# Optimization experiments

Hardware: AMD Instinct MI355X
Metric: run time of the kernel (lower is better)

The kernel has to match this reference:

```python
import jax, jax.numpy as jnp
import numpy as np

H = 4
D = 64          # attention_head_size
HID = H * D     # 256
LN_EPS = 1e-12


def setup_inputs() -> dict:
    key = jax.random.key(0)
    ks = jax.random.split(key, 20)
    B, S = 8, 200
    s = 0.02
    inp = {
        'input_tensor': jax.random.normal(ks[0], (B, S, HID), jnp.float32),
        'attention_mask': jnp.zeros((B, 1, S, S), jnp.float32),
        'absolute_pos_K': jax.random.normal(ks[1], (B, S, HID), jnp.float32),
        'absolute_pos_V': jax.random.normal(ks[2], (B, S, HID), jnp.float32),
        'time_matrix_emb_K': jax.random.normal(ks[3], (B, S, S, HID), jnp.float32),
        'time_matrix_emb_V': jax.random.normal(ks[4], (B, S, S, HID), jnp.float32),
        'Wq': jax.random.normal(ks[5], (HID, HID), jnp.float32) * s,
        'bq': jnp.zeros((HID,), jnp.float32),
        'Wk': jax.random.normal(ks[6], (HID, HID), jnp.float32) * s,
        'bk': jnp.zeros((HID,), jnp.float32),
        'Wv': jax.random.normal(ks[7], (HID, HID), jnp.float32) * s,
        'bv': jnp.zeros((HID,), jnp.float32),
        'order_w': jax.random.normal(ks[8], (2 * D,), jnp.float32) * s,
        'order_b': jnp.zeros((), jnp.float32),
        'dist_w': jax.random.normal(ks[9], (2 * D,), jnp.float32) * s,
        'dist_b': jnp.zeros((), jnp.float32),
        'scalar': jax.random.normal(ks[10], (1,), jnp.float32),
        'Wd': jax.random.normal(ks[11], (HID, HID), jnp.float32) * s,
        'bd': jnp.zeros((HID,), jnp.float32),
        'ln_g': jnp.ones((HID,), jnp.float32),
        'ln_b': jnp.zeros((HID,), jnp.float32),
    }
    return inp


def _forward(input_tensor, attention_mask, absolute_pos_K, absolute_pos_V,
             time_matrix_emb_K, time_matrix_emb_V,
             Wq, bq, Wk, bk, Wv, bv, order_w, order_b, dist_w, dist_b,
             scalar, Wd, bd, ln_g, ln_b):
    B, S, _ = input_tensor.shape
    heads = lambda x: x.reshape(B, S, H, D).transpose(0, 2, 1, 3)  # -> [B,H,S,D]
    q = heads(input_tensor @ Wq + bq)
    k = heads(input_tensor @ Wk + bk)
    v = heads(input_tensor @ Wv + bv)
    posK = heads(absolute_pos_K)                                   # [B,H,S,D]
    posV = heads(absolute_pos_V)
    timeK = time_matrix_emb_K.reshape(B, S, S, H, D).transpose(0, 3, 1, 2, 4)  # [B,H,S,S,D]
    timeV = time_matrix_emb_V.reshape(B, S, S, H, D).transpose(0, 3, 1, 2, 4)

    scores = (jnp.einsum('bhid,bhjd->bhij', q, k)
              + jnp.einsum('bhid,bhjd->bhij', q, posK)
              + jnp.einsum('bhijd,bhid->bhij', timeK, q))          # [B,H,S,S]

    # order_affine(cat(q_i,k_j)) == q_i@w[:D] + k_j@w[D:] + b (Linear on concat)
    pr_order = jax.nn.sigmoid(jnp.einsum('bhid,d->bhi', q, order_w[:D])[:, :, :, None]
                              + jnp.einsum('bhjd,d->bhj', k, order_w[D:])[:, :, None, :]
                              + order_b)
    gd_order = jnp.triu(jnp.ones((S, S), jnp.float32), 1)[None, None]
    error_order = (jnp.log(pr_order + 1e-24) * gd_order
                   + jnp.log(1.0 - pr_order + 1e-24) * (1.0 - gd_order))

    idx = jnp.arange(S, dtype=jnp.float32)
    gd_dist = jnp.log(jnp.abs(idx[None, :] - idx[:, None]) + 1.0)[None, None]
    pr_dist = (jnp.einsum('bhid,d->bhi', q, dist_w[:D])[:, :, :, None]
               + jnp.einsum('bhjd,d->bhj', k, dist_w[D:])[:, :, None, :]
               + dist_b)
    error_distance = -jnp.square(gd_dist - pr_dist) * jnp.square(scalar[0]) / 2.0

    scores = scores + error_order + error_distance
    probs = jax.nn.softmax(scores / np.sqrt(D) + attention_mask, axis=-1)

    ctx = (jnp.einsum('bhij,bhjd->bhid', probs, v)
           + jnp.einsum('bhij,bhjd->bhid', probs, posV)
           + jnp.einsum('bhij,bhijd->bhid', probs, timeV))
    ctx = ctx.transpose(0, 2, 1, 3).reshape(B, S, HID)

    hs = ctx @ Wd + bd + input_tensor
    mu = jnp.mean(hs, axis=-1, keepdims=True)
    var = jnp.mean(jnp.square(hs - mu), axis=-1, keepdims=True)
    return (hs - mu) / jnp.sqrt(var + LN_EPS) * ln_g + ln_b


def reference(input_tensor, attention_mask, absolute_pos_K, absolute_pos_V,
              time_matrix_emb_K, time_matrix_emb_V,
              Wq, bq, Wk, bk, Wv, bv, order_w, order_b, dist_w, dist_b,
              scalar, Wd, bd, ln_g, ln_b):
    return _forward(input_tensor, attention_mask, absolute_pos_K, absolute_pos_V,
                    time_matrix_emb_K, time_matrix_emb_V,
                    Wq, bq, Wk, bk, Wv, bv, order_w, order_b, dist_w, dist_b,
                    scalar, Wd, bd, ln_g, ln_b)
```

## Files before the change

kernel.cpp:

```cpp
#include <hip/hip_runtime.h>

#define SB 8
#define SS 200
#define HID 256
#define NH 4
#define DH 64

__global__ __launch_bounds__(256) void proj_kernel(
    const float* __restrict__ in,
    const float* __restrict__ Wq, const float* __restrict__ bq,
    const float* __restrict__ Wk, const float* __restrict__ bk,
    const float* __restrict__ Wv, const float* __restrict__ bv,
    const float* __restrict__ posK, const float* __restrict__ posV,
    float* __restrict__ q_out, float* __restrict__ k_out,
    float* __restrict__ kpk_out, float* __restrict__ vpv_out)
{
    const int which = blockIdx.y;
    const float* W = (which == 0) ? Wq : (which == 1) ? Wk : Wv;
    const float* bias = (which == 0) ? bq : (which == 1) ? bk : bv;
    const int row0 = blockIdx.x * 16;
    __shared__ float sin_[16][HID];
    const int t = threadIdx.x;
    for (int r = 0; r < 16; r++)
        sin_[r][t] = in[(size_t)(row0 + r) * HID + t];
    __syncthreads();
    const int tx = t & 63, ty = t >> 6;
    const int c0 = tx * 4, r0 = ty * 4;
    float acc[4][4] = {};
    for (int kk = 0; kk < HID; kk++) {
        const float4 wv4 = *(const float4*)(W + (size_t)kk * HID + c0);
        float a[4];
        #pragma unroll
        for (int r = 0; r < 4; r++) a[r] = sin_[r0 + r][kk];
        #pragma unroll
        for (int r = 0; r < 4; r++) {
            acc[r][0] += a[r] * wv4.x;
            acc[r][1] += a[r] * wv4.y;
            acc[r][2] += a[r] * wv4.z;
            acc[r][3] += a[r] * wv4.w;
        }
    }
    const float4 b4 = *(const float4*)(bias + c0);
    #pragma unroll
    for (int r = 0; r < 4; r++) {
        const size_t off = (size_t)(row0 + r0 + r) * HID + c0;
        float4 o;
        o.x = acc[r][0] + b4.x;
        o.y = acc[r][1] + b4.y;
        o.z = acc[r][2] + b4.z;
        o.w = acc[r][3] + b4.w;
        if (which == 0) {
            *(float4*)(q_out + off) = o;
        } else if (which == 1) {
            *(float4*)(k_out + off) = o;
            const float4 p4 = *(const float4*)(posK + off);
            float4 s;
            s.x = o.x + p4.x; s.y = o.y + p4.y;
            s.z = o.z + p4.z; s.w = o.w + p4.w;
            *(float4*)(kpk_out + off) = s;
        } else {
            const float4 p4 = *(const float4*)(posV + off);
            float4 s;
            s.x = o.x + p4.x; s.y = o.y + p4.y;
            s.z = o.z + p4.z; s.w = o.w + p4.w;
            *(float4*)(vpv_out + off) = s;
        }
    }
}

__global__ __launch_bounds__(64) void rowdots_kernel(
    const float* __restrict__ q, const float* __restrict__ k,
    const float* __restrict__ order_w, const float* __restrict__ dist_w,
    float* __restrict__ qo, float* __restrict__ ko,
    float* __restrict__ qd, float* __restrict__ kd)
{
    const int row = blockIdx.x;
    const int l = threadIdx.x;
    const float ow1 = order_w[l], ow2 = order_w[64 + l];
    const float dw1 = dist_w[l],  dw2 = dist_w[64 + l];
    for (int h = 0; h < NH; h++) {
        const float qe = q[(size_t)row * HID + h * DH + l];
        const float ke = k[(size_t)row * HID + h * DH + l];
        float a = qe * ow1, b = ke * ow2, c = qe * dw1, d = ke * dw2;
        #pragma unroll
        for (int m = 32; m >= 1; m >>= 1) {
            a += __shfl_xor(a, m, 64);
            b += __shfl_xor(b, m, 64);
            c += __shfl_xor(c, m, 64);
            d += __shfl_xor(d, m, 64);
        }
        if (l == 0) {
            qo[row * NH + h] = a;
            ko[row * NH + h] = b;
            qd[row * NH + h] = c;
            kd[row * NH + h] = d;
        }
    }
}

__global__ __launch_bounds__(256) void attn_kernel(
    const float* __restrict__ q, const float* __restrict__ kpk,
    const float* __restrict__ vpv,
    const float* __restrict__ timeK, const float* __restrict__ timeV,
    const float* __restrict__ mask,
    const float* __restrict__ qo, const float* __restrict__ ko,
    const float* __restrict__ qd, const float* __restrict__ kd,
    const float* __restrict__ order_b_p, const float* __restrict__ dist_b_p,
    const float* __restrict__ scalar_p,
    float* __restrict__ ctx)
{
    const int blk = blockIdx.x;
    const int b = blk / SS, i = blk - b * SS;
    const int t = threadIdx.x;
    const int w = t >> 6, l = t & 63;
    const int h = l >> 4;
    const int sub = l & 15;

    __shared__ float sh_q[HID];
    __shared__ float sh_s[NH][SS + 8];
    __shared__ float sh_red[4][HID];

    const size_t rowq = (size_t)blk * HID;
    sh_q[t] = q[rowq + t];
    __syncthreads();

    const int d0 = l * 4;
    const float4 qr = *(const float4*)(sh_q + d0);

    const float qo_h = qo[blk * NH + h];
    const float qd_h = qd[blk * NH + h];
    const float order_b = *order_b_p;
    const float dist_b = *dist_b_p;
    const float sc = *scalar_p;
    const float sc2h = 0.5f * sc * sc;
    const size_t tb = (size_t)blk * SS;

    for (int j0 = 0; j0 < SS; j0 += 4) {
        const int j = j0 + w;
        const float4 tk = *(const float4*)(timeK + (tb + j) * (size_t)HID + d0);
        const float4 kk = *(const float4*)(kpk + ((size_t)(b * SS + j)) * HID + d0);
        float part = (tk.x + kk.x) * qr.x + (tk.y + kk.y) * qr.y
                   + (tk.z + kk.z) * qr.z + (tk.w + kk.w) * qr.w;
        part += __shfl_xor(part, 1, 64);
        part += __shfl_xor(part, 2, 64);
        part += __shfl_xor(part, 4, 64);
        part += __shfl_xor(part, 8, 64);
        if (sub == 0) {
            const float ko_jh = ko[(b * SS + j) * NH + h];
            const float kd_jh = kd[(b * SS + j) * NH + h];
            const float xo = qo_h + ko_jh + order_b;
            const float pr = 1.0f / (1.0f + __expf(-xo));
            const float eo = (j > i) ? __logf(pr + 1e-24f) : __logf(1.0f - pr + 1e-24f);
            const float xd = qd_h + kd_jh + dist_b;
            const float gd = __logf(fabsf((float)(i - j)) + 1.0f);
            const float dd = gd - xd;
            const float ed = -dd * dd * sc2h;
            const float mk = mask[tb + j];
            sh_s[h][j] = (part + eo + ed) * 0.125f + mk;
        }
    }
    __syncthreads();

    {
        float vals[4];
        float m = -1e30f;
        #pragma unroll
        for (int rep = 0; rep < 4; rep++) {
            const int j = l + rep * 64;
            vals[rep] = (j < SS) ? sh_s[w][j] : -1e30f;
            m = fmaxf(m, vals[rep]);
        }
        #pragma unroll
        for (int mm = 32; mm >= 1; mm >>= 1) m = fmaxf(m, __shfl_xor(m, mm, 64));
        float sum = 0.0f;
        float es[4];
        #pragma unroll
        for (int rep = 0; rep < 4; rep++) {
            const int j = l + rep * 64;
            if (j < SS) { es[rep] = __expf(vals[rep] - m); sum += es[rep]; }
        }
        #pragma unroll
        for (int mm = 32; mm >= 1; mm >>= 1) sum += __shfl_xor(sum, mm, 64);
        const float inv = 1.0f / sum;
        #pragma unroll
        for (int rep = 0; rep < 4; rep++) {
            const int j = l + rep * 64;
            if (j < SS) sh_s[w][j] = es[rep] * inv;
        }
    }
    __syncthreads();

    float4 acc = make_float4(0.f, 0.f, 0.f, 0.f);
    for (int j0 = 0; j0 < SS; j0 += 4) {
        const int j = j0 + w;
        const float4 tv = *(const float4*)(timeV + (tb + j) * (size_t)HID + d0);
        const float4 vv = *(const float4*)(vpv + ((size_t)(b * SS + j)) * HID + d0);
        const float p = sh_s[h][j];
        acc.x += p * (tv.x + vv.x);
        acc.y += p * (tv.y + vv.y);
        acc.z += p * (tv.z + vv.z);
        acc.w += p * (tv.w + vv.w);
    }
    *(float4*)(&sh_red[w][d0]) = acc;
    __syncthreads();
    ctx[rowq + t] = sh_red[0][t] + sh_red[1][t] + sh_red[2][t] + sh_red[3][t];
}

__global__ __launch_bounds__(256) void outproj_kernel(
    const float* __restrict__ ctx, const float* __restrict__ Wd,
    const float* __restrict__ bd, const float* __restrict__ input,
    float* __restrict__ hs)
{
    const int row0 = blockIdx.x * 16;
    __shared__ float sin_[16][HID];
    const int t = threadIdx.x;
    for (int r = 0; r < 16; r++)
        sin_[r][t] = ctx[(size_t)(row0 + r) * HID + t];
    __syncthreads();
    const int tx = t & 63, ty = t >> 6;
    const int c0 = tx * 4, r0 = ty * 4;
    float acc[4][4] = {};
    for (int kk = 0; kk < HID; kk++) {
        const float4 wv4 = *(const float4*)(Wd + (size_t)kk * HID + c0);
        float a[4];
        #pragma unroll
        for (int r = 0; r < 4; r++) a[r] = sin_[r0 + r][kk];
        #pragma unroll
        for (int r = 0; r < 4; r++) {
            acc[r][0] += a[r] * wv4.x;
            acc[r][1] += a[r] * wv4.y;
            acc[r][2] += a[r] * wv4.z;
            acc[r][3] += a[r] * wv4.w;
        }
    }
    const float4 b4 = *(const float4*)(bd + c0);
    #pragma unroll
    for (int r = 0; r < 4; r++) {
        const size_t off = (size_t)(row0 + r0 + r) * HID + c0;
        const float4 i4 = *(const float4*)(input + off);
        float4 o;
        o.x = acc[r][0] + b4.x + i4.x;
        o.y = acc[r][1] + b4.y + i4.y;
        o.z = acc[r][2] + b4.z + i4.z;
        o.w = acc[r][3] + b4.w + i4.w;
        *(float4*)(hs + off) = o;
    }
}

__global__ __launch_bounds__(256) void ln_kernel(
    const float* __restrict__ hs, const float* __restrict__ g,
    const float* __restrict__ be, float* __restrict__ out)
{
    const int row = blockIdx.x;
    const int t = threadIdx.x;
    const int w = t >> 6, l = t & 63;
    __shared__ float red[4];
    const float v = hs[(size_t)row * HID + t];
    float s = v;
    #pragma unroll
    for (int m = 32; m >= 1; m >>= 1) s += __shfl_xor(s, m, 64);
    if (l == 0) red[w] = s;
    __syncthreads();
    const float mu = (red[0] + red[1] + red[2] + red[3]) * (1.0f / 256.0f);
    __syncthreads();
    const float d = v - mu;
    float s2 = d * d;
    #pragma unroll
    for (int m = 32; m >= 1; m >>= 1) s2 += __shfl_xor(s2, m, 64);
    if (l == 0) red[w] = s2;
    __syncthreads();
    const float var = (red[0] + red[1] + red[2] + red[3]) * (1.0f / 256.0f);
    out[(size_t)row * HID + t] = d * rsqrtf(var + 1e-12f) * g[t] + be[t];
}

extern "C" void kernel_launch(void* const* d_in, const int* in_sizes, int n_in,
                              void* d_out, int out_size, void* d_ws, size_t ws_size,
                              hipStream_t stream) {
    const float* input   = (const float*)d_in[0];
    const float* mask    = (const float*)d_in[1];
    const float* posK    = (const float*)d_in[2];
    const float* posV    = (const float*)d_in[3];
    const float* timeK   = (const float*)d_in[4];
    const float* timeV   = (const float*)d_in[5];
    const float* Wq      = (const float*)d_in[6];
    const float* bq      = (const float*)d_in[7];
    const float* Wk      = (const float*)d_in[8];
    const float* bk      = (const float*)d_in[9];
    const float* Wv      = (const float*)d_in[10];
    const float* bv      = (const float*)d_in[11];
    const float* order_w = (const float*)d_in[12];
    const float* order_b = (const float*)d_in[13];
    const float* dist_w  = (const float*)d_in[14];
    const float* dist_b  = (const float*)d_in[15];
    const float* scalar  = (const float*)d_in[16];
    const float* Wd      = (const float*)d_in[17];
    const float* bd      = (const float*)d_in[18];
    const float* ln_g    = (const float*)d_in[19];
    const float* ln_b    = (const float*)d_in[20];

    const int NROW = SB * SS;
    float* ws = (float*)d_ws;
    float* q_ws   = ws;
    float* k_ws   = q_ws   + 409600;
    float* kpk_ws = k_ws   + 409600;
    float* vpv_ws = kpk_ws + 409600;
    float* qo_ws  = vpv_ws + 409600;
    float* ko_ws  = qo_ws  + 6400;
    float* qd_ws  = ko_ws  + 6400;
    float* kd_ws  = qd_ws  + 6400;
    float* ctx_ws = kd_ws  + 6400;
    float* hs_ws  = ctx_ws + 409600;

    proj_kernel<<<dim3(NROW / 16, 3), 256, 0, stream>>>(
        input, Wq, bq, Wk, bk, Wv, bv, posK, posV,
        q_ws, k_ws, kpk_ws, vpv_ws);
    rowdots_kernel<<<NROW, 64, 0, stream>>>(
        q_ws, k_ws, order_w, dist_w, qo_ws, ko_ws, qd_ws, kd_ws);
    attn_kernel<<<NROW, 256, 0, stream>>>(
        q_ws, kpk_ws, vpv_ws, timeK, timeV, mask,
        qo_ws, ko_ws, qd_ws, kd_ws, order_b, dist_b, scalar, ctx_ws);
    outproj_kernel<<<NROW / 16, 256, 0, stream>>>(
        ctx_ws, Wd, bd, input, hs_ws);
    ln_kernel<<<NROW, 256, 0, stream>>>(
        hs_ws, ln_g, ln_b, (float*)d_out);
}
```

Measured before the change: 742.2 us.

## Fuse rowdots into projection and out-proj plus layernorm into attention

Folds the order/distance row-dot reductions into the QKV projection epilogue and folds the output projection, residual and layer norm into the attention kernel, cutting five launches to two and removing intermediate buffers. Per-key order/distance error terms are precomputed into shared memory before the score loop. The time-embedding streams use nontemporal loads and the key loops are unrolled by two for more loads in flight. The fused per-row output projection rereads Wd from cache in every block, which adds some compute per block.

```diff
diff --git a/kernel.cpp b/kernel.cpp
--- a/kernel.cpp
+++ b/kernel.cpp
@@ -6,58 +6,102 @@
 #define NH 4
 #define DH 64
 
-__global__ __launch_bounds__(256) void proj_kernel(
+typedef float f32x4_t __attribute__((ext_vector_type(4)));
+
+__device__ __forceinline__ float4 ntload4(const float* p) {
+    f32x4_t v = __builtin_nontemporal_load((const f32x4_t*)p);
+    return make_float4(v.x, v.y, v.z, v.w);
+}
+
+__global__ __launch_bounds__(256) void proj_fused_kernel(
     const float* __restrict__ in,
     const float* __restrict__ Wq, const float* __restrict__ bq,
     const float* __restrict__ Wk, const float* __restrict__ bk,
     const float* __restrict__ Wv, const float* __restrict__ bv,
     const float* __restrict__ posK, const float* __restrict__ posV,
-    float* __restrict__ q_out, float* __restrict__ k_out,
-    float* __restrict__ kpk_out, float* __restrict__ vpv_out)
+    const float* __restrict__ order_w, const float* __restrict__ dist_w,
+    float* __restrict__ q_out, float* __restrict__ kpk_out,
+    float* __restrict__ vpv_out,
+    float* __restrict__ qo, float* __restrict__ ko,
+    float* __restrict__ qd, float* __restrict__ kd)
 {
     const int which = blockIdx.y;
     const float* W = (which == 0) ? Wq : (which == 1) ? Wk : Wv;
     const float* bias = (which == 0) ? bq : (which == 1) ? bk : bv;
-    const int row0 = blockIdx.x * 16;
-    __shared__ float sin_[16][HID];
+    const int row0 = blockIdx.x * 8;
+    __shared__ float sin_[8][HID];
     const int t = threadIdx.x;
-    for (int r = 0; r < 16; r++)
+    #pragma unroll
+    for (int r = 0; r < 8; r++)
         sin_[r][t] = in[(size_t)(row0 + r) * HID + t];
     __syncthreads();
+
     const int tx = t & 63, ty = t >> 6;
-    const int c0 = tx * 4, r0 = ty * 4;
-    float acc[4][4] = {};
+    const int c0 = tx * 4, r0 = ty * 2;
+    float acc[2][4] = {};
+    #pragma unroll 4
     for (int kk = 0; kk < HID; kk++) {
         const float4 wv4 = *(const float4*)(W + (size_t)kk * HID + c0);
-        float a[4];
-        #pragma unroll
-        for (int r = 0; r < 4; r++) a[r] = sin_[r0 + r][kk];
-        #pragma unroll
-        for (int r = 0; r < 4; r++) {
-            acc[r][0] += a[r] * wv4.x;
-            acc[r][1] += a[r] * wv4.y;
-            acc[r][2] += a[r] * wv4.z;
-            acc[r][3] += a[r] * wv4.w;
-        }
-    }
+        const float a0 = sin_[r0][kk];
+        const float a1 = sin_[r0 + 1][kk];
+        acc[0][0] += a0 * wv4.x; acc[0][1] += a0 * wv4.y;
+        acc[0][2] += a0 * wv4.z; acc[0][3] += a0 * wv4.w;
+        acc[1][0] += a1 * wv4.x; acc[1][1] += a1 * wv4.y;
+        acc[1][2] += a1 * wv4.z; acc[1][3] += a1 * wv4.w;
+    }
+
     const float4 b4 = *(const float4*)(bias + c0);
-    #pragma unroll
-    for (int r = 0; r < 4; r++) {
-        const size_t off = (size_t)(row0 + r0 + r) * HID + c0;
+    const int hh = tx >> 4;
+    const int dd4 = (tx & 15) * 4;
+    float4 ow4 = make_float4(0.f, 0.f, 0.f, 0.f);
+    float4 dw4 = make_float4(0.f, 0.f, 0.f, 0.f);
+    if (which == 0) {
+        ow4 = *(const float4*)(order_w + dd4);
+        dw4 = *(const float4*)(dist_w + dd4);
+    } else if (which == 1) {
+        ow4 = *(const float4*)(order_w + 64 + dd4);
+        dw4 = *(const float4*)(dist_w + 64 + dd4);
+    }
+
+    #pragma unroll
+    for (int rr = 0; rr < 2; rr++) {
+        const int row = row0 + r0 + rr;
+        const size_t off = (size_t)row * HID + c0;
         float4 o;
-        o.x = acc[r][0] + b4.x;
-        o.y = acc[r][1] + b4.y;
-        o.z = acc[r][2] + b4.z;
-        o.w = acc[r][3] + b4.w;
+        o.x = acc[rr][0] + b4.x;
+        o.y = acc[rr][1] + b4.y;
+        o.z = acc[rr][2] + b4.z;
+        o.w = acc[rr][3] + b4.w;
         if (which == 0) {
             *(float4*)(q_out + off) = o;
+            float po = o.x * ow4.x + o.y * ow4.y + o.z * ow4.z + o.w * ow4.w;
+            float pd = o.x * dw4.x + o.y * dw4.y + o.z * dw4.z + o.w * dw4.w;
+            #pragma unroll
+            for (int m = 1; m <= 8; m <<= 1) {
+                po += __shfl_xor(po, m, 64);
+                pd += __shfl_xor(pd, m, 64);
+            }
+            if ((tx & 15) == 0) {
+                qo[row * NH + hh] = po;
+                qd[row * NH + hh] = pd;
+            }
         } else if (which == 1) {
-            *(float4*)(k_out + off) = o;
             const float4 p4 = *(const float4*)(posK + off);
             float4 s;
             s.x = o.x + p4.x; s.y = o.y + p4.y;
             s.z = o.z + p4.z; s.w = o.w + p4.w;
             *(float4*)(kpk_out + off) = s;
+            float po = o.x * ow4.x + o.y * ow4.y + o.z * ow4.z + o.w * ow4.w;
+            float pd = o.x * dw4.x + o.y * dw4.y + o.z * dw4.z + o.w * dw4.w;
+            #pragma unroll
+            for (int m = 1; m <= 8; m <<= 1) {
+                po += __shfl_xor(po, m, 64);
+                pd += __shfl_xor(pd, m, 64);
+            }
+            if ((tx & 15) == 0) {
+                ko[row * NH + hh] = po;
+                kd[row * NH + hh] = pd;
+            }
         } else {
             const float4 p4 = *(const float4*)(posV + off);
             float4 s;
@@ -68,37 +112,7 @@
     }
 }
 
-__global__ __launch_bounds__(64) void rowdots_kernel(
-    const float* __restrict__ q, const float* __restrict__ k,
-    const float* __restrict__ order_w, const float* __restrict__ dist_w,
-    float* __restrict__ qo, float* __restrict__ ko,
-    float* __restrict__ qd, float* __restrict__ kd)
-{
-    const int row = blockIdx.x;
-    const int l = threadIdx.x;
-    const float ow1 = order_w[l], ow2 = order_w[64 + l];
-    const float dw1 = dist_w[l],  dw2 = dist_w[64 + l];
-    for (int h = 0; h < NH; h++) {
-        const float qe = q[(size_t)row * HID + h * DH + l];
-        const float ke = k[(size_t)row * HID + h * DH + l];
-        float a = qe * ow1, b = ke * ow2, c = qe * dw1, d = ke * dw2;
-        #pragma unroll
-        for (int m = 32; m >= 1; m >>= 1) {
-            a += __shfl_xor(a, m, 64);
-            b += __shfl_xor(b, m, 64);
-            c += __shfl_xor(c, m, 64);
-            d += __shfl_xor(d, m, 64);
-        }
-        if (l == 0) {
-            qo[row * NH + h] = a;
-            ko[row * NH + h] = b;
-            qd[row * NH + h] = c;
-            kd[row * NH + h] = d;
-        }
-    }
-}
-
-__global__ __launch_bounds__(256) void attn_kernel(
+__global__ __launch_bounds__(256) void attn_fused_kernel(
     const float* __restrict__ q, const float* __restrict__ kpk,
     const float* __restrict__ vpv,
     const float* __restrict__ timeK, const float* __restrict__ timeV,
@@ -107,7 +121,10 @@
     const float* __restrict__ qd, const float* __restrict__ kd,
     const float* __restrict__ order_b_p, const float* __restrict__ dist_b_p,
     const float* __restrict__ scalar_p,
-    float* __restrict__ ctx)
+    const float* __restrict__ Wd, const float* __restrict__ bd,
+    const float* __restrict__ input,
+    const float* __restrict__ ln_g, const float* __restrict__ ln_b,
+    float* __restrict__ out)
 {
     const int blk = blockIdx.x;
     const int b = blk / SS, i = blk - b * SS;
@@ -117,46 +134,52 @@
     const int sub = l & 15;
 
     __shared__ float sh_q[HID];
+    __shared__ float sh_e[NH][SS + 8];
     __shared__ float sh_s[NH][SS + 8];
     __shared__ float sh_red[4][HID];
+    __shared__ float sh_c[HID];
+    __shared__ float red2[4];
 
     const size_t rowq = (size_t)blk * HID;
     sh_q[t] = q[rowq + t];
-    __syncthreads();
-
-    const int d0 = l * 4;
-    const float4 qr = *(const float4*)(sh_q + d0);
-
-    const float qo_h = qo[blk * NH + h];
-    const float qd_h = qd[blk * NH + h];
+
     const float order_b = *order_b_p;
     const float dist_b = *dist_b_p;
     const float sc = *scalar_p;
     const float sc2h = 0.5f * sc * sc;
     const size_t tb = (size_t)blk * SS;
-
-    for (int j0 = 0; j0 < SS; j0 += 4) {
-        const int j = j0 + w;
-        const float4 tk = *(const float4*)(timeK + (tb + j) * (size_t)HID + d0);
-        const float4 kk = *(const float4*)(kpk + ((size_t)(b * SS + j)) * HID + d0);
-        float part = (tk.x + kk.x) * qr.x + (tk.y + kk.y) * qr.y
-                   + (tk.z + kk.z) * qr.z + (tk.w + kk.w) * qr.w;
-        part += __shfl_xor(part, 1, 64);
-        part += __shfl_xor(part, 2, 64);
-        part += __shfl_xor(part, 4, 64);
-        part += __shfl_xor(part, 8, 64);
+    for (int idx = t; idx < NH * SS; idx += 256) {
+        const int eh = idx & 3, j = idx >> 2;
+        const float xo = qo[blk * NH + eh] + ko[(b * SS + j) * NH + eh] + order_b;
+        const float pr = 1.0f / (1.0f + __expf(-xo));
+        const float eo = (j > i) ? __logf(pr + 1e-24f) : __logf(1.0f - pr + 1e-24f);
+        const float xd = qd[blk * NH + eh] + kd[(b * SS + j) * NH + eh] + dist_b;
+        const float gd = __logf(fabsf((float)(i - j)) + 1.0f);
+        const float dv = gd - xd;
+        sh_e[eh][j] = (eo - dv * dv * sc2h) * 0.125f + mask[tb + j];
+    }
+    __syncthreads();
+
+    const int d0 = l * 4;
+    const float4 qr = *(const float4*)(sh_q + d0);
+
+    for (int j0 = 0; j0 < SS; j0 += 8) {
+        const int ja = j0 + w, jb = ja + 4;
+        const float4 ta = ntload4(timeK + (tb + ja) * (size_t)HID + d0);
+        const float4 tb4 = ntload4(timeK + (tb + jb) * (size_t)HID + d0);
+        const float4 ka = *(const float4*)(kpk + ((size_t)(b * SS + ja)) * HID + d0);
+        const float4 kb = *(const float4*)(kpk + ((size_t)(b * SS + jb)) * HID + d0);
+        float pa = (ta.x + ka.x) * qr.x + (ta.y + ka.y) * qr.y
+                 + (ta.z + ka.z) * qr.z + (ta.w + ka.w) * qr.w;
+        float pb = (tb4.x + kb.x) * qr.x + (tb4.y + kb.y) * qr.y
+                 + (tb4.z + kb.z) * qr.z + (tb4.w + kb.w) * qr.w;
+        pa += __shfl_xor(pa, 1, 64); pb += __shfl_xor(pb, 1, 64);
+        pa += __shfl_xor(pa, 2, 64); pb += __shfl_xor(pb, 2, 64);
+        pa += __shfl_xor(pa, 4, 64); pb += __shfl_xor(pb, 4, 64);
+        pa += __shfl_xor(pa, 8, 64); pb += __shfl_xor(pb, 8, 64);
         if (sub == 0) {
-            const float ko_jh = ko[(b * SS + j) * NH + h];
-            const float kd_jh = kd[(b * SS + j) * NH + h];
-            const float xo = qo_h + ko_jh + order_b;
-            const float pr = 1.0f / (1.0f + __expf(-xo));
-            const float eo = (j > i) ? __logf(pr + 1e-24f) : __logf(1.0f - pr + 1e-24f);
-            const float xd = qd_h + kd_jh + dist_b;
-            const float gd = __logf(fabsf((float)(i - j)) + 1.0f);
-            const float dd = gd - xd;
-            const float ed = -dd * dd * sc2h;
-            const float mk = mask[tb + j];
-            sh_s[h][j] = (part + eo + ed) * 0.125f + mk;
+            sh_s[h][ja] = pa * 0.125f + sh_e[h][ja];
+            sh_s[h][jb] = pb * 0.125f + sh_e[h][jb];
         }
     }
     __syncthreads();
@@ -191,86 +214,44 @@
     __syncthreads();
 
     float4 acc = make_float4(0.f, 0.f, 0.f, 0.f);
-    for (int j0 = 0; j0 < SS; j0 += 4) {
-        const int j = j0 + w;
-        const float4 tv = *(const float4*)(timeV + (tb + j) * (size_t)HID + d0);
-        const float4 vv = *(const float4*)(vpv + ((size_t)(b * SS + j)) * HID + d0);
-        const float p = sh_s[h][j];
-        acc.x += p * (tv.x + vv.x);
-        acc.y += p * (tv.y + vv.y);
-        acc.z += p * (tv.z + vv.z);
-        acc.w += p * (tv.w + vv.w);
+    for (int j0 = 0; j0 < SS; j0 += 8) {
+        const int ja = j0 + w, jb = ja + 4;
+        const float4 ta = ntload4(timeV + (tb + ja) * (size_t)HID + d0);
+        const float4 tb4 = ntload4(timeV + (tb + jb) * (size_t)HID + d0);
+        const float4 va = *(const float4*)(vpv + ((size_t)(b * SS + ja)) * HID + d0);
+        const float4 vb = *(const float4*)(vpv + ((size_t)(b * SS + jb)) * HID + d0);
+        const float pa = sh_s[h][ja];
+        const float pb = sh_s[h][jb];
+        acc.x += pa * (ta.x + va.x) + pb * (tb4.x + vb.x);
+        acc.y += pa * (ta.y + va.y) + pb * (tb4.y + vb.y);
+        acc.z += pa * (ta.z + va.z) + pb * (tb4.z + vb.z);
+        acc.w += pa * (ta.w + va.w) + pb * (tb4.w + vb.w);
     }
     *(float4*)(&sh_red[w][d0]) = acc;
     __syncthreads();
-    ctx[rowq + t] = sh_red[0][t] + sh_red[1][t] + sh_red[2][t] + sh_red[3][t];
-}
-
-__global__ __launch_bounds__(256) void outproj_kernel(
-    const float* __restrict__ ctx, const float* __restrict__ Wd,
-    const float* __restrict__ bd, const float* __restrict__ input,
-    float* __restrict__ hs)
-{
-    const int row0 = blockIdx.x * 16;
-    __shared__ float sin_[16][HID];
-    const int t = threadIdx.x;
-    for (int r = 0; r < 16; r++)
-        sin_[r][t] = ctx[(size_t)(row0 + r) * HID + t];
-    __syncthreads();
-    const int tx = t & 63, ty = t >> 6;
-    const int c0 = tx * 4, r0 = ty * 4;
-    float acc[4][4] = {};
-    for (int kk = 0; kk < HID; kk++) {
-        const float4 wv4 = *(const float4*)(Wd + (size_t)kk * HID + c0);
-        float a[4];
-        #pragma unroll
-        for (int r = 0; r < 4; r++) a[r] = sin_[r0 + r][kk];
-        #pragma unroll
-        for (int r = 0; r < 4; r++) {
-            acc[r][0] += a[r] * wv4.x;
-            acc[r][1] += a[r] * wv4.y;
-            acc[r][2] += a[r] * wv4.z;
-            acc[r][3] += a[r] * wv4.w;
-        }
-    }
-    const float4 b4 = *(const float4*)(bd + c0);
-    #pragma unroll
-    for (int r = 0; r < 4; r++) {
-        const size_t off = (size_t)(row0 + r0 + r) * HID + c0;
-        const float4 i4 = *(const float4*)(input + off);
-        float4 o;
-        o.x = acc[r][0] + b4.x + i4.x;
-        o.y = acc[r][1] + b4.y + i4.y;
-        o.z = acc[r][2] + b4.z + i4.z;
-        o.w = acc[r][3] + b4.w + i4.w;
-        *(float4*)(hs + off) = o;
-    }
-}
-
-__global__ __launch_bounds__(256) void ln_kernel(
-    const float* __restrict__ hs, const float* __restrict__ g,
-    const float* __restrict__ be, float* __restrict__ out)
-{
-    const int row = blockIdx.x;
-    const int t = threadIdx.x;
-    const int w = t >> 6, l = t & 63;
-    __shared__ float red[4];
-    const float v = hs[(size_t)row * HID + t];
-    float s = v;
+    sh_c[t] = sh_red[0][t] + sh_red[1][t] + sh_red[2][t] + sh_red[3][t];
+    __syncthreads();
+
+    float hsv = bd[t] + input[rowq + t];
+    #pragma unroll 4
+    for (int kk = 0; kk < HID; kk++)
+        hsv += sh_c[kk] * Wd[(size_t)kk * HID + t];
+
+    float s = hsv;
     #pragma unroll
     for (int m = 32; m >= 1; m >>= 1) s += __shfl_xor(s, m, 64);
-    if (l == 0) red[w] = s;
-    __syncthreads();
-    const float mu = (red[0] + red[1] + red[2] + red[3]) * (1.0f / 256.0f);
-    __syncthreads();
-    const float d = v - mu;
-    float s2 = d * d;
+    if (l == 0) red2[w] = s;
+    __syncthreads();
+    const float mu = (red2[0] + red2[1] + red2[2] + red2[3]) * (1.0f / 256.0f);
+    __syncthreads();
+    const float dv = hsv - mu;
+    float s2 = dv * dv;
     #pragma unroll
     for (int m = 32; m >= 1; m >>= 1) s2 += __shfl_xor(s2, m, 64);
-    if (l == 0) red[w] = s2;
-    __syncthreads();
-    const float var = (red[0] + red[1] + red[2] + red[3]) * (1.0f / 256.0f);
-    out[(size_t)row * HID + t] = d * rsqrtf(var + 1e-12f) * g[t] + be[t];
+    if (l == 0) red2[w] = s2;
+    __syncthreads();
+    const float var = (red2[0] + red2[1] + red2[2] + red2[3]) * (1.0f / 256.0f);
+    out[rowq + t] = dv * rsqrtf(var + 1e-12f) * ln_g[t] + ln_b[t];
 }
 
 extern "C" void kernel_launch(void* const* d_in, const int* in_sizes, int n_in,
@@ -301,26 +282,18 @@
     const int NROW = SB * SS;
     float* ws = (float*)d_ws;
     float* q_ws   = ws;
-    float* k_ws   = q_ws   + 409600;
-    float* kpk_ws = k_ws   + 409600;
+    float* kpk_ws = q_ws   + 409600;
     float* vpv_ws = kpk_ws + 409600;
     float* qo_ws  = vpv_ws + 409600;
     float* ko_ws  = qo_ws  + 6400;
     float* qd_ws  = ko_ws  + 6400;
     float* kd_ws  = qd_ws  + 6400;
-    float* ctx_ws = kd_ws  + 6400;
-    float* hs_ws  = ctx_ws + 409600;
-
-    proj_kernel<<<dim3(NROW / 16, 3), 256, 0, stream>>>(
-        input, Wq, bq, Wk, bk, Wv, bv, posK, posV,
-        q_ws, k_ws, kpk_ws, vpv_ws);
-    rowdots_kernel<<<NROW, 64, 0, stream>>>(
-        q_ws, k_ws, order_w, dist_w, qo_ws, ko_ws, qd_ws, kd_ws);
-    attn_kernel<<<NROW, 256, 0, stream>>>(
+
+    proj_fused_kernel<<<dim3(NROW / 8, 3), 256, 0, stream>>>(
+        input, Wq, bq, Wk, bk, Wv, bv, posK, posV, order_w, dist_w,
+        q_ws, kpk_ws, vpv_ws, qo_ws, ko_ws, qd_ws, kd_ws);
+    attn_fused_kernel<<<NROW, 256, 0, stream>>>(
         q_ws, kpk_ws, vpv_ws, timeK, timeV, mask,
-        qo_ws, ko_ws, qd_ws, kd_ws, order_b, dist_b, scalar, ctx_ws);
-    outproj_kernel<<<NROW / 16, 256, 0, stream>>>(
-        ctx_ws, Wd, bd, input, hs_ws);
-    ln_kernel<<<NROW, 256, 0, stream>>>(
-        hs_ws, ln_g, ln_b, (float*)d_out);
-}
+        qo_ws, ko_ws, qd_ws, kd_ws, order_b, dist_b, scalar,
+        Wd, bd, input, ln_g, ln_b, (float*)d_out);
+}
```

Result: faster. 697.6 us (-6.0%).
